# Kernel optimization log

Hardware: AMD Instinct MI355X
Metric: run time of the kernel (lower is better)

The kernel has to match this reference:

```python
import jax, jax.numpy as jnp
import numpy as np

B, S, H = 4, 1024, 1024
NH = 16
D = H // NH  # attention_head_size = 64
L = 9        # num_labels
MAXREL = 5
B_PERSON = 1
I_PERSON = 2
LN_EPS = 1e-5


def setup_inputs() -> dict:
    key = jax.random.key(0)
    ks = jax.random.split(key, 16)
    lin = lambda k, i, o: 0.02 * jax.random.normal(k, (i, o), jnp.float32)
    return {
        "sequence_output": jax.random.normal(ks[0], (B, S, H), jnp.float32),
        "Wq": lin(ks[1], H, H), "bq": jnp.zeros((H,), jnp.float32),
        "Wk": lin(ks[2], H, H), "bk": jnp.zeros((H,), jnp.float32),
        "Wv": lin(ks[3], H, H), "bv": jnp.zeros((H,), jnp.float32),
        "Wo": lin(ks[4], H, H), "bo": jnp.zeros((H,), jnp.float32),
        "ln_g": jnp.ones((H,), jnp.float32), "ln_b": jnp.zeros((H,), jnp.float32),
        "Ws": lin(ks[5], H, L), "bs": jnp.zeros((L,), jnp.float32),
        "entity_bias": 0.1 * jax.random.normal(ks[6], (L,), jnp.float32),
        "rel_pos_emb": jax.random.normal(ks[7], (2 * MAXREL + 1, D), jnp.float32),  # declared but unused in forward math, matching the torch module
    }


def reference(sequence_output, Wq, bq, Wk, bk, Wv, bv, Wo, bo, ln_g, ln_b, Ws, bs, entity_bias, rel_pos_emb):
    x = sequence_output  # [B,S,H]
    b, s, _ = x.shape

    def heads(t):  # [B,S,H] -> [B,NH,S,D]
        return t.reshape(b, s, NH, D).transpose(0, 2, 1, 3)

    q = heads(x @ Wq + bq)
    k = heads(x @ Wk + bk)
    v = heads(x @ Wv + bv)

    scores = jnp.einsum('bhqd,bhkd->bhqk', q, k)  # [B,NH,S,S]

    r = jnp.arange(s, dtype=jnp.float32)
    dist = jnp.abs(r[:, None] - r[None, :])                 # |i-j|, [S,S]
    pos_bias = jnp.exp(-0.1 * jnp.clip(dist, 0.0, float(MAXREL)))
    # torch order: (scores + pos_bias) / sqrt(D) + distance_mask
    scores = (scores + pos_bias) / np.sqrt(D) + (-0.1) * dist

    probs = jax.nn.softmax(scores, axis=-1)  # dropout is identity in eval
    ctx = jnp.einsum('bhqk,bhkd->bhqd', probs, v)
    ctx = ctx.transpose(0, 2, 1, 3).reshape(b, s, H)

    y = x + (ctx @ Wo + bo)  # residual
    mu = y.mean(-1, keepdims=True)
    var = y.var(-1, keepdims=True)
    yn = (y - mu) / jnp.sqrt(var + LN_EPS) * ln_g + ln_b

    span_logits = yn @ Ws + bs  # [B,S,L]
    # entity-bias loop: if argmax(span_logits[i,j-1]) == B-PERSON, add entity_bias[I-PERSON] twice to final[i,j,I-PERSON]
    prev_is_b = (jnp.argmax(span_logits[:, :-1, :], axis=-1) == B_PERSON).astype(span_logits.dtype)  # [B,S-1]
    final_logits = span_logits.at[:, 1:, I_PERSON].add(2.0 * entity_bias[I_PERSON] * prev_is_b)
    return final_logits
```

## Files before the change

kernel.cpp:

```cpp
#include <hip/hip_runtime.h>
#include <hip/hip_bf16.h>
#include <math.h>

typedef unsigned short ush;
typedef __attribute__((ext_vector_type(8))) _Float16 fragh;
typedef __attribute__((ext_vector_type(4))) _Float16 half4;
typedef __attribute__((ext_vector_type(4))) float f32x4;

#define S_   1024
#define H_   1024
#define NH_  16
#define D_   64
#define L_   9
#define MB_  (1048576ull)

__device__ __forceinline__ void load_lds16(const ush* g, const ush* l) {
  __builtin_amdgcn_global_load_lds(
      (const __attribute__((address_space(1))) void*)g,
      (__attribute__((address_space(3))) void*)l, 16, 0, 0);
}

__global__ __launch_bounds__(256) void cast_wT4(
    const float* W0, const float* W1, const float* W2, const float* W3,
    ush* T0, ush* T1, ush* T2, ush* T3) {
  __shared__ __align__(16) float Ls[64][68];
  const float* W = (blockIdx.z == 0) ? W0 : (blockIdx.z == 1) ? W1
                 : (blockIdx.z == 2) ? W2 : W3;
  ush* Th = (blockIdx.z == 0) ? T0 : (blockIdx.z == 1) ? T1
          : (blockIdx.z == 2) ? T2 : T3;
  const int tid = threadIdx.x;
  const int n0 = blockIdx.x * 64, k0 = blockIdx.y * 64;
#pragma unroll
  for (int it = 0; it < 4; it++) {
    int flat = tid + 256 * it;
    int row = flat >> 4, nc = (flat & 15) * 4;
    *(float4*)&Ls[row][nc] = *(const float4*)&W[(size_t)(k0 + row) * 1024 + n0 + nc];
  }
  __syncthreads();
#pragma unroll
  for (int it = 0; it < 2; it++) {
    int flat = tid + 256 * it;
    int nrow = flat >> 3, kc = (flat & 7) * 8;
    fragh v;
#pragma unroll
    for (int u = 0; u < 8; u++) v[u] = (_Float16)Ls[kc + u][nrow];
    *(fragh*)&Th[(size_t)(n0 + nrow) * 1024 + k0 + kc] = v;
  }
}

__global__ __launch_bounds__(256) void cast_x(
    const float* __restrict__ x, ush* __restrict__ xh) {
  const size_t i = ((size_t)blockIdx.x * 256 + threadIdx.x) * 8;
  float4 a = *(const float4*)&x[i];
  float4 b = *(const float4*)&x[i + 4];
  fragh v;
  v[0] = (_Float16)a.x; v[1] = (_Float16)a.y;
  v[2] = (_Float16)a.z; v[3] = (_Float16)a.w;
  v[4] = (_Float16)b.x; v[5] = (_Float16)b.y;
  v[6] = (_Float16)b.z; v[7] = (_Float16)b.w;
  *(fragh*)&xh[i] = v;
}

__global__ __launch_bounds__(256) void gemm_qkv(
    const ush* __restrict__ xh,
    const ush* __restrict__ Bq, const ush* __restrict__ Bk,
    const ush* __restrict__ Bv,
    const float* __restrict__ bq, const float* __restrict__ bk,
    const float* __restrict__ bv,
    ush* __restrict__ qh, ush* __restrict__ kh, ush* __restrict__ vT) {
  __shared__ __align__(16) ush As[2][128][32];
  __shared__ __align__(16) ush Bs[2][128][32];
  const int tid = threadIdx.x, lane = tid & 63, wave = tid >> 6;
  const int l15 = lane & 15, quad = lane >> 4;
  const int m0 = blockIdx.y * 128, n0 = blockIdx.x * 128;
  const int z = blockIdx.z;
  const ush* Bg = (z == 0) ? Bq : (z == 1) ? Bk : Bv;
  const float* bias = (z == 0) ? bq : (z == 1) ? bk : bv;
  ush* outp = (z == 0) ? qh : (z == 1) ? kh : vT;

  const int wm = (wave >> 1) * 64, wn = (wave & 1) * 64;

  f32x4 acc[4][4];
#pragma unroll
  for (int i = 0; i < 4; i++)
#pragma unroll
    for (int j = 0; j < 4; j++) acc[i][j] = (f32x4){0.f, 0.f, 0.f, 0.f};

  auto stage = [&](int bi, int k0) {
#pragma unroll
    for (int jj = 0; jj < 2; jj++) {
      const int call = wave * 2 + jj;
      const int c = call * 64 + lane;
      const int r = c >> 2, ch = c & 3;
      load_lds16(xh + (size_t)(m0 + r) * 1024 + k0 + ch * 8,
                 &As[bi][0][0] + (size_t)call * 512);
    }
#pragma unroll
    for (int jj = 0; jj < 2; jj++) {
      const int call = wave * 2 + jj;
      const int c = call * 64 + lane;
      const int r = c >> 2, ch = c & 3;
      load_lds16(Bg + (size_t)(n0 + r) * 1024 + k0 + ch * 8,
                 &Bs[bi][0][0] + (size_t)call * 512);
    }
  };

  auto compute = [&](int cur) {
    fragh a[4], b[2][2];
#pragma unroll
    for (int s = 0; s < 4; s++)
      a[s] = *(const fragh*)&As[cur][wm + s * 16 + l15][quad * 8];
#pragma unroll
    for (int t = 0; t < 4; t++) {
      fragh bt = *(const fragh*)&Bs[cur][wn + t * 16 + l15][quad * 8];
#pragma unroll
      for (int mi = 0; mi < 4; mi++)
        acc[mi][t] = __builtin_amdgcn_mfma_f32_16x16x32_f16(
            a[mi], bt, acc[mi][t], 0, 0, 0);
    }
    (void)b;
  };

  stage(0, 0);
#pragma unroll 1
  for (int t = 0; t < 31; ++t) {
    const int cur = t & 1;
    stage(cur ^ 1, (t + 1) << 5);
    __builtin_amdgcn_sched_barrier(0);
    asm volatile("s_waitcnt vmcnt(4)" ::: "memory");
    __builtin_amdgcn_sched_barrier(0);
    __builtin_amdgcn_s_barrier();
    compute(cur);
    __builtin_amdgcn_s_barrier();
  }
  __builtin_amdgcn_sched_barrier(0);
  asm volatile("s_waitcnt vmcnt(0)" ::: "memory");
  __builtin_amdgcn_sched_barrier(0);
  __builtin_amdgcn_s_barrier();
  compute(1);

#pragma unroll
  for (int mi = 0; mi < 4; mi++) {
    const int rbase = m0 + wm + mi * 16 + quad * 4;
    const int bb = rbase >> 10, ss = rbase & 1023;
#pragma unroll
    for (int ni = 0; ni < 4; ni++) {
      const int col = n0 + wn + ni * 16 + l15;
      const float bv_ = bias[col];
      const int hidx = col >> 6, d = col & 63;
      if (z == 2) {
        half4 p4;
        p4[0] = (_Float16)(acc[mi][ni][0] + bv_);
        p4[1] = (_Float16)(acc[mi][ni][1] + bv_);
        p4[2] = (_Float16)(acc[mi][ni][2] + bv_);
        p4[3] = (_Float16)(acc[mi][ni][3] + bv_);
        *(half4*)&outp[((size_t)(bb * NH_ + hidx) * D_ + d) * S_ + ss] = p4;
      } else {
#pragma unroll
        for (int r = 0; r < 4; r++) {
          const size_t o =
              ((size_t)(bb * NH_ + hidx) * S_ + (ss + r)) * D_ + d;
          *(_Float16*)&outp[o] = (_Float16)(acc[mi][ni][r] + bv_);
        }
      }
    }
  }
}

__global__ __launch_bounds__(256) void gemm_o(
    const ush* __restrict__ ctxh, const ush* __restrict__ Bo,
    const float* __restrict__ bo, const float* __restrict__ resid,
    float* __restrict__ outf) {
  __shared__ __align__(16) ush As[2][128][32];
  __shared__ __align__(16) ush Bs[2][64][32];
  const int tid = threadIdx.x, lane = tid & 63, wave = tid >> 6;
  const int l15 = lane & 15, quad = lane >> 4;
  const int m0 = blockIdx.y * 128, n0 = blockIdx.x * 64;
  const int wm = (wave >> 1) * 64, wn = (wave & 1) * 32;

  f32x4 acc[4][2];
#pragma unroll
  for (int i = 0; i < 4; i++)
#pragma unroll
    for (int j = 0; j < 2; j++) acc[i][j] = (f32x4){0.f, 0.f, 0.f, 0.f};

  auto stage = [&](int bi, int k0) {
#pragma unroll
    for (int jj = 0; jj < 2; jj++) {
      const int call = wave * 2 + jj;
      const int c = call * 64 + lane;
      const int r = c >> 2, ch = c & 3;
      load_lds16(ctxh + (size_t)(m0 + r) * 1024 + k0 + ch * 8,
                 &As[bi][0][0] + (size_t)call * 512);
    }
    {
      const int c = wave * 64 + lane;
      const int r = c >> 2, ch = c & 3;
      load_lds16(Bo + (size_t)(n0 + r) * 1024 + k0 + ch * 8,
                 &Bs[bi][0][0] + (size_t)wave * 512);
    }
  };

  auto compute = [&](int cur) {
    fragh a[4], b[2];
#pragma unroll
    for (int s = 0; s < 4; s++)
      a[s] = *(const fragh*)&As[cur][wm + s * 16 + l15][quad * 8];
#pragma unroll
    for (int t = 0; t < 2; t++)
      b[t] = *(const fragh*)&Bs[cur][wn + t * 16 + l15][quad * 8];
#pragma unroll
    for (int mi = 0; mi < 4; mi++)
#pragma unroll
      for (int ni = 0; ni < 2; ni++)
        acc[mi][ni] = __builtin_amdgcn_mfma_f32_16x16x32_f16(
            a[mi], b[ni], acc[mi][ni], 0, 0, 0);
  };

  stage(0, 0);
#pragma unroll 1
  for (int t = 0; t < 31; ++t) {
    const int cur = t & 1;
    stage(cur ^ 1, (t + 1) << 5);
    __builtin_amdgcn_sched_barrier(0);
    asm volatile("s_waitcnt vmcnt(3)" ::: "memory");
    __builtin_amdgcn_sched_barrier(0);
    __builtin_amdgcn_s_barrier();
    compute(cur);
    __builtin_amdgcn_s_barrier();
  }
  __builtin_amdgcn_sched_barrier(0);
  asm volatile("s_waitcnt vmcnt(0)" ::: "memory");
  __builtin_amdgcn_sched_barrier(0);
  __builtin_amdgcn_s_barrier();
  compute(1);

#pragma unroll
  for (int mi = 0; mi < 4; mi++) {
    const int rbase = m0 + wm + mi * 16 + quad * 4;
#pragma unroll
    for (int ni = 0; ni < 2; ni++) {
      const int col = n0 + wn + ni * 16 + l15;
      const float bv_ = bo[col];
#pragma unroll
      for (int r = 0; r < 4; r++) {
        const int m = rbase + r;
        outf[(size_t)m * 1024 + col] =
            acc[mi][ni][r] + bv_ + resid[(size_t)m * 1024 + col];
      }
    }
  }
}

__global__ __launch_bounds__(256) void attn2(
    const ush* __restrict__ qh, const ush* __restrict__ kh,
    const ush* __restrict__ vT, ush* __restrict__ ch) {
  __shared__ __align__(16) ush Kh[64][72];
  __shared__ __align__(16) ush VTs[64][72];
  __shared__ __align__(16) ush Pst[64][72];
  __shared__ float LUT[256];
  const int tid = threadIdx.x;
  const int lane = tid & 63, wave = tid >> 6;
  const int l15 = lane & 15, quad = lane >> 4;
  const int w16 = wave * 16;
  const int bh = blockIdx.y;
  const int b = bh >> 4, h = bh & 15;
  const int q0 = blockIdx.x * 64;

  const float K1 = 0.18033688011112042f;
  const float K2 = 0.14426950408889634f;
  {
    const float dd = (float)tid;
    LUT[tid] = __expf(-0.1f * fminf(dd, 5.0f)) * K1 - dd * K2
             - 2.8853900817779268f;
  }

  const size_t qrow = ((size_t)bh * S_ + q0 + w16 + l15) * D_;
  fragh a_h[2];
  a_h[0] = *(const fragh*)&qh[qrow + quad * 8];
  a_h[1] = *(const fragh*)&qh[qrow + 32 + quad * 8];

  f32x4 o[4];
  float lrow[4];
#pragma unroll
  for (int i = 0; i < 4; i++) {
    o[i] = (f32x4){0.f, 0.f, 0.f, 0.f};
    lrow[i] = 0.f;
  }

  const size_t kbase = (size_t)bh * S_ * D_;
  const size_t vbase = (size_t)bh * D_ * S_;

  const int jlo = (q0 > 128) ? q0 - 128 : 0;
  const int jend = (q0 + 192 < S_) ? q0 + 192 : S_;

  for (int j0 = jlo; j0 < jend; j0 += 64) {
    __syncthreads();
#pragma unroll
    for (int it = 0; it < 2; it++) {
      const int flat = tid + 256 * it;
      const int row = flat >> 3, dc = (flat & 7) * 8;
      *(uint4*)&Kh[row][dc] =
          *(const uint4*)&kh[kbase + (size_t)(j0 + row) * D_ + dc];
      *(uint4*)&VTs[row][dc] =
          *(const uint4*)&vT[vbase + (size_t)row * S_ + j0 + dc];
    }
    __syncthreads();

    f32x4 c4[4];
#pragma unroll
    for (int nt = 0; nt < 4; nt++) c4[nt] = (f32x4){0.f, 0.f, 0.f, 0.f};
#pragma unroll
    for (int kk = 0; kk < 2; kk++) {
#pragma unroll
      for (int nt = 0; nt < 4; nt++) {
        fragh bh_ = *(const fragh*)&Kh[nt * 16 + l15][kk * 32 + quad * 8];
        c4[nt] = __builtin_amdgcn_mfma_f32_16x16x32_f16(a_h[kk], bh_, c4[nt], 0, 0, 0);
      }
    }

    const int ib = q0 + w16 + quad * 4 - j0 - l15;
#pragma unroll
    for (int r = 0; r < 4; r++) {
#pragma unroll
      for (int nt = 0; nt < 4; nt++) {
        int di = ib + r - nt * 16;
        di = (di < 0) ? -di : di;
        const float sv = exp2f(fmaf(c4[nt][r], K1, LUT[di]));
        lrow[r] += sv;
        *(_Float16*)&Pst[w16 + quad * 4 + r][nt * 16 + l15] = (_Float16)sv;
      }
    }

    fragh pa[2];
    pa[0] = *(const fragh*)&Pst[w16 + l15][quad * 8];
    pa[1] = *(const fragh*)&Pst[w16 + l15][32 + quad * 8];
#pragma unroll
    for (int dt = 0; dt < 4; dt++) {
      fragh vb0 = *(const fragh*)&VTs[dt * 16 + l15][quad * 8];
      fragh vb1 = *(const fragh*)&VTs[dt * 16 + l15][32 + quad * 8];
      o[dt] = __builtin_amdgcn_mfma_f32_16x16x32_f16(pa[0], vb0, o[dt], 0, 0, 0);
      o[dt] = __builtin_amdgcn_mfma_f32_16x16x32_f16(pa[1], vb1, o[dt], 0, 0, 0);
    }
  }

#pragma unroll
  for (int r = 0; r < 4; r++) {
#pragma unroll
    for (int off = 1; off < 16; off <<= 1) lrow[r] += __shfl_xor(lrow[r], off);
    const float inv = 1.0f / lrow[r];
    const size_t rowp =
        ((size_t)(b * S_ + q0 + w16 + quad * 4 + r)) * H_ + h * 64;
#pragma unroll
    for (int dt = 0; dt < 4; dt++)
      *(_Float16*)&ch[rowp + dt * 16 + l15] = (_Float16)(o[dt][r] * inv);
  }
}

__global__ __launch_bounds__(256) void ln_span(
    const float* __restrict__ y, const float* __restrict__ g,
    const float* __restrict__ bta, const float* __restrict__ Wsp,
    const float* __restrict__ bs, float* __restrict__ logits) {
  const int row = blockIdx.x;
  const int tid = threadIdx.x, lane = tid & 63, wave = tid >> 6;
  const float* yr = y + (size_t)row * 1024;
  float vals[4], s = 0.f, s2 = 0.f;
#pragma unroll
  for (int i = 0; i < 4; i++) {
    float t = yr[tid + i * 256];
    vals[i] = t; s += t; s2 += t * t;
  }
#pragma unroll
  for (int off = 32; off; off >>= 1) {
    s += __shfl_xor(s, off);
    s2 += __shfl_xor(s2, off);
  }
  __shared__ float red[8];
  __shared__ float red9[4][12];
  if (lane == 0) { red[wave] = s; red[4 + wave] = s2; }
  __syncthreads();
  s = red[0] + red[1] + red[2] + red[3];
  s2 = red[4] + red[5] + red[6] + red[7];
  const float mu = s * (1.0f / 1024.0f);
  const float var = s2 * (1.0f / 1024.0f) - mu * mu;
  const float inv = rsqrtf(var + 1e-5f);

  float lg[9];
#pragma unroll
  for (int l = 0; l < 9; l++) lg[l] = 0.f;
#pragma unroll
  for (int i = 0; i < 4; i++) {
    const int hh = tid + i * 256;
    const float yn = (vals[i] - mu) * inv * g[hh] + bta[hh];
#pragma unroll
    for (int l = 0; l < 9; l++) lg[l] += yn * Wsp[hh * 9 + l];
  }
#pragma unroll
  for (int l = 0; l < 9; l++) {
#pragma unroll
    for (int off = 32; off; off >>= 1) lg[l] += __shfl_xor(lg[l], off);
  }
  if (lane == 0) {
#pragma unroll
    for (int l = 0; l < 9; l++) red9[wave][l] = lg[l];
  }
  __syncthreads();
  if (tid < 9) {
    logits[(size_t)row * 9 + tid] =
        red9[0][tid] + red9[1][tid] + red9[2][tid] + red9[3][tid] + bs[tid];
  }
}

__global__ __launch_bounds__(256) void final_kernel(
    const float* __restrict__ logits, const float* __restrict__ eb,
    float* __restrict__ out) {
  const int m = blockIdx.x * 256 + threadIdx.x;
  const int i = m & 1023;
  float cur[9];
#pragma unroll
  for (int l = 0; l < 9; l++) cur[l] = logits[(size_t)m * 9 + l];
  if (i > 0) {
    const float* prev = logits + (size_t)(m - 1) * 9;
    int am = 0;
    float best = prev[0];
#pragma unroll
    for (int l = 1; l < 9; l++) {
      float pv = prev[l];
      if (pv > best) { best = pv; am = l; }
    }
    if (am == 1) cur[2] += 2.0f * eb[2];
  }
#pragma unroll
  for (int l = 0; l < 9; l++) out[(size_t)m * 9 + l] = cur[l];
}

extern "C" void kernel_launch(void* const* d_in, const int* in_sizes, int n_in,
                              void* d_out, int out_size, void* d_ws, size_t ws_size,
                              hipStream_t stream) {
  const float* x    = (const float*)d_in[0];
  const float* Wq   = (const float*)d_in[1];
  const float* bq   = (const float*)d_in[2];
  const float* Wk   = (const float*)d_in[3];
  const float* bk   = (const float*)d_in[4];
  const float* Wv   = (const float*)d_in[5];
  const float* bv   = (const float*)d_in[6];
  const float* Wo   = (const float*)d_in[7];
  const float* bo   = (const float*)d_in[8];
  const float* ln_g = (const float*)d_in[9];
  const float* ln_b = (const float*)d_in[10];
  const float* Ws   = (const float*)d_in[11];
  const float* bs   = (const float*)d_in[12];
  const float* eb   = (const float*)d_in[13];
  float* out = (float*)d_out;
  char* W8 = (char*)d_ws;

  ush* WoT  = (ush*)(W8 + 0 * MB_);
  ush* WqT  = (ush*)(W8 + 2 * MB_);
  ush* WkT  = (ush*)(W8 + 4 * MB_);
  ush* WvT  = (ush*)(W8 + 6 * MB_);
  ush* xh   = (ush*)(W8 + 8 * MB_);
  ush* qh   = (ush*)(W8 + 16 * MB_);
  ush* kh   = (ush*)(W8 + 24 * MB_);
  ush* vT   = (ush*)(W8 + 32 * MB_);
  ush* ctxh = (ush*)(W8 + 40 * MB_);
  float* y_ws  = (float*)(W8 + 48 * MB_);
  float* lg_ws = (float*)(W8 + 16 * MB_);

  cast_wT4<<<dim3(16, 16, 4), 256, 0, stream>>>(
      Wq, Wk, Wv, Wo, WqT, WkT, WvT, WoT);
  cast_x<<<2048, 256, 0, stream>>>(x, xh);

  gemm_qkv<<<dim3(8, 32, 3), 256, 0, stream>>>(
      xh, WqT, WkT, WvT, bq, bk, bv, qh, kh, vT);
  attn2<<<dim3(16, 64), 256, 0, stream>>>(qh, kh, vT, ctxh);
  gemm_o<<<dim3(16, 32), 256, 0, stream>>>(ctxh, WoT, bo, x, y_ws);
  ln_span<<<4096, 256, 0, stream>>>(y_ws, ln_g, ln_b, Ws, bs, lg_ws);
  final_kernel<<<16, 256, 0, stream>>>(lg_ws, eb, out);
}
```

Measured before the change: 203.0 us.

## Merge prep casts, store residual output in fp16, warp-per-row LayerNorm, add setprio

The x cast, weight transposes and a new Ws transpose are combined into one prep launch. The output projection now writes the residual sum as fp16, halving the y traffic read by LayerNorm. LayerNorm+span is rewritten to one wave per row with vectorized loads and no block barriers. The attention MFMA sections are wrapped with s_setprio. Storing y in fp16 before LayerNorm slightly reduces precision.

```diff
diff --git a/kernel.cpp b/kernel.cpp
--- a/kernel.cpp
+++ b/kernel.cpp
@@ -20,45 +20,56 @@
       (__attribute__((address_space(3))) void*)l, 16, 0, 0);
 }
 
-__global__ __launch_bounds__(256) void cast_wT4(
+__global__ __launch_bounds__(256) void prep(
+    const float* __restrict__ x,
     const float* W0, const float* W1, const float* W2, const float* W3,
-    ush* T0, ush* T1, ush* T2, ush* T3) {
+    const float* __restrict__ Ws,
+    ush* __restrict__ xh, ush* T0, ush* T1, ush* T2, ush* T3,
+    float* __restrict__ WsT) {
   __shared__ __align__(16) float Ls[64][68];
-  const float* W = (blockIdx.z == 0) ? W0 : (blockIdx.z == 1) ? W1
-                 : (blockIdx.z == 2) ? W2 : W3;
-  ush* Th = (blockIdx.z == 0) ? T0 : (blockIdx.z == 1) ? T1
-          : (blockIdx.z == 2) ? T2 : T3;
+  const int bid = blockIdx.x;
   const int tid = threadIdx.x;
-  const int n0 = blockIdx.x * 64, k0 = blockIdx.y * 64;
+
+  if (bid < 2048) {
+    const size_t i = ((size_t)bid * 256 + tid) * 8;
+    float4 a = *(const float4*)&x[i];
+    float4 b = *(const float4*)&x[i + 4];
+    fragh v;
+    v[0] = (_Float16)a.x; v[1] = (_Float16)a.y;
+    v[2] = (_Float16)a.z; v[3] = (_Float16)a.w;
+    v[4] = (_Float16)b.x; v[5] = (_Float16)b.y;
+    v[6] = (_Float16)b.z; v[7] = (_Float16)b.w;
+    *(fragh*)&xh[i] = v;
+    return;
+  }
+  if (bid >= 3072) {
+    for (int idx = tid; idx < 1024 * 9; idx += 256) {
+      const int r = idx / 9, c = idx - r * 9;
+      WsT[c * 1024 + r] = Ws[idx];
+    }
+    return;
+  }
+  const int flat = bid - 2048;
+  const int wz = flat >> 8, wy = (flat >> 4) & 15, wx = flat & 15;
+  const float* W = (wz == 0) ? W0 : (wz == 1) ? W1 : (wz == 2) ? W2 : W3;
+  ush* Th = (wz == 0) ? T0 : (wz == 1) ? T1 : (wz == 2) ? T2 : T3;
+  const int n0 = wx * 64, k0 = wy * 64;
 #pragma unroll
   for (int it = 0; it < 4; it++) {
-    int flat = tid + 256 * it;
-    int row = flat >> 4, nc = (flat & 15) * 4;
+    int f = tid + 256 * it;
+    int row = f >> 4, nc = (f & 15) * 4;
     *(float4*)&Ls[row][nc] = *(const float4*)&W[(size_t)(k0 + row) * 1024 + n0 + nc];
   }
   __syncthreads();
 #pragma unroll
   for (int it = 0; it < 2; it++) {
-    int flat = tid + 256 * it;
-    int nrow = flat >> 3, kc = (flat & 7) * 8;
+    int f = tid + 256 * it;
+    int nrow = f >> 3, kc = (f & 7) * 8;
     fragh v;
 #pragma unroll
     for (int u = 0; u < 8; u++) v[u] = (_Float16)Ls[kc + u][nrow];
     *(fragh*)&Th[(size_t)(n0 + nrow) * 1024 + k0 + kc] = v;
   }
-}
-
-__global__ __launch_bounds__(256) void cast_x(
-    const float* __restrict__ x, ush* __restrict__ xh) {
-  const size_t i = ((size_t)blockIdx.x * 256 + threadIdx.x) * 8;
-  float4 a = *(const float4*)&x[i];
-  float4 b = *(const float4*)&x[i + 4];
-  fragh v;
-  v[0] = (_Float16)a.x; v[1] = (_Float16)a.y;
-  v[2] = (_Float16)a.z; v[3] = (_Float16)a.w;
-  v[4] = (_Float16)b.x; v[5] = (_Float16)b.y;
-  v[6] = (_Float16)b.z; v[7] = (_Float16)b.w;
-  *(fragh*)&xh[i] = v;
 }
 
 __global__ __launch_bounds__(256) void gemm_qkv(
@@ -106,7 +117,7 @@
   };
 
   auto compute = [&](int cur) {
-    fragh a[4], b[2][2];
+    fragh a[4];
 #pragma unroll
     for (int s = 0; s < 4; s++)
       a[s] = *(const fragh*)&As[cur][wm + s * 16 + l15][quad * 8];
@@ -118,7 +129,6 @@
         acc[mi][t] = __builtin_amdgcn_mfma_f32_16x16x32_f16(
             a[mi], bt, acc[mi][t], 0, 0, 0);
     }
-    (void)b;
   };
 
   stage(0, 0);
@@ -170,7 +180,7 @@
 __global__ __launch_bounds__(256) void gemm_o(
     const ush* __restrict__ ctxh, const ush* __restrict__ Bo,
     const float* __restrict__ bo, const float* __restrict__ resid,
-    float* __restrict__ outf) {
+    ush* __restrict__ yh) {
   __shared__ __align__(16) ush As[2][128][32];
   __shared__ __align__(16) ush Bs[2][64][32];
   const int tid = threadIdx.x, lane = tid & 63, wave = tid >> 6;
@@ -245,8 +255,9 @@
 #pragma unroll
       for (int r = 0; r < 4; r++) {
         const int m = rbase + r;
-        outf[(size_t)m * 1024 + col] =
+        const float val =
             acc[mi][ni][r] + bv_ + resid[(size_t)m * 1024 + col];
+        *(_Float16*)&yh[(size_t)m * 1024 + col] = (_Float16)val;
       }
     }
   }
@@ -310,6 +321,7 @@
     f32x4 c4[4];
 #pragma unroll
     for (int nt = 0; nt < 4; nt++) c4[nt] = (f32x4){0.f, 0.f, 0.f, 0.f};
+    __builtin_amdgcn_s_setprio(1);
 #pragma unroll
     for (int kk = 0; kk < 2; kk++) {
 #pragma unroll
@@ -318,6 +330,7 @@
         c4[nt] = __builtin_amdgcn_mfma_f32_16x16x32_f16(a_h[kk], bh_, c4[nt], 0, 0, 0);
       }
     }
+    __builtin_amdgcn_s_setprio(0);
 
     const int ib = q0 + w16 + quad * 4 - j0 - l15;
 #pragma unroll
@@ -335,6 +348,7 @@
     fragh pa[2];
     pa[0] = *(const fragh*)&Pst[w16 + l15][quad * 8];
     pa[1] = *(const fragh*)&Pst[w16 + l15][32 + quad * 8];
+    __builtin_amdgcn_s_setprio(1);
 #pragma unroll
     for (int dt = 0; dt < 4; dt++) {
       fragh vb0 = *(const fragh*)&VTs[dt * 16 + l15][quad * 8];
@@ -342,6 +356,7 @@
       o[dt] = __builtin_amdgcn_mfma_f32_16x16x32_f16(pa[0], vb0, o[dt], 0, 0, 0);
       o[dt] = __builtin_amdgcn_mfma_f32_16x16x32_f16(pa[1], vb1, o[dt], 0, 0, 0);
     }
+    __builtin_amdgcn_s_setprio(0);
   }
 
 #pragma unroll
@@ -358,56 +373,64 @@
 }
 
 __global__ __launch_bounds__(256) void ln_span(
-    const float* __restrict__ y, const float* __restrict__ g,
-    const float* __restrict__ bta, const float* __restrict__ Wsp,
+    const ush* __restrict__ yh, const float* __restrict__ g,
+    const float* __restrict__ bta, const float* __restrict__ WsT,
     const float* __restrict__ bs, float* __restrict__ logits) {
-  const int row = blockIdx.x;
   const int tid = threadIdx.x, lane = tid & 63, wave = tid >> 6;
-  const float* yr = y + (size_t)row * 1024;
-  float vals[4], s = 0.f, s2 = 0.f;
-#pragma unroll
-  for (int i = 0; i < 4; i++) {
-    float t = yr[tid + i * 256];
-    vals[i] = t; s += t; s2 += t * t;
-  }
+  const int row = blockIdx.x * 4 + wave;
+  const int h0 = lane * 16;
+  const ush* yr = yh + (size_t)row * 1024 + h0;
+
+  fragh v0 = *(const fragh*)yr;
+  fragh v1 = *(const fragh*)(yr + 8);
+  float v[16];
+#pragma unroll
+  for (int u = 0; u < 8; u++) { v[u] = (float)v0[u]; v[8 + u] = (float)v1[u]; }
+
+  float s = 0.f, s2 = 0.f;
+#pragma unroll
+  for (int u = 0; u < 16; u++) { s += v[u]; s2 += v[u] * v[u]; }
 #pragma unroll
   for (int off = 32; off; off >>= 1) {
     s += __shfl_xor(s, off);
     s2 += __shfl_xor(s2, off);
   }
-  __shared__ float red[8];
-  __shared__ float red9[4][12];
-  if (lane == 0) { red[wave] = s; red[4 + wave] = s2; }
-  __syncthreads();
-  s = red[0] + red[1] + red[2] + red[3];
-  s2 = red[4] + red[5] + red[6] + red[7];
   const float mu = s * (1.0f / 1024.0f);
   const float var = s2 * (1.0f / 1024.0f) - mu * mu;
   const float inv = rsqrtf(var + 1e-5f);
 
+  float yn[16];
+#pragma unroll
+  for (int i = 0; i < 4; i++) {
+    float4 gg = *(const float4*)&g[h0 + i * 4];
+    float4 bb = *(const float4*)&bta[h0 + i * 4];
+    yn[i * 4 + 0] = (v[i * 4 + 0] - mu) * inv * gg.x + bb.x;
+    yn[i * 4 + 1] = (v[i * 4 + 1] - mu) * inv * gg.y + bb.y;
+    yn[i * 4 + 2] = (v[i * 4 + 2] - mu) * inv * gg.z + bb.z;
+    yn[i * 4 + 3] = (v[i * 4 + 3] - mu) * inv * gg.w + bb.w;
+  }
+
   float lg[9];
 #pragma unroll
-  for (int l = 0; l < 9; l++) lg[l] = 0.f;
-#pragma unroll
-  for (int i = 0; i < 4; i++) {
-    const int hh = tid + i * 256;
-    const float yn = (vals[i] - mu) * inv * g[hh] + bta[hh];
-#pragma unroll
-    for (int l = 0; l < 9; l++) lg[l] += yn * Wsp[hh * 9 + l];
-  }
-#pragma unroll
   for (int l = 0; l < 9; l++) {
+    float acc = 0.f;
+#pragma unroll
+    for (int i = 0; i < 4; i++) {
+      float4 w4 = *(const float4*)&WsT[l * 1024 + h0 + i * 4];
+      acc += yn[i * 4 + 0] * w4.x + yn[i * 4 + 1] * w4.y +
+             yn[i * 4 + 2] * w4.z + yn[i * 4 + 3] * w4.w;
+    }
+    lg[l] = acc;
+  }
+#pragma unroll
+  for (int l = 0; l < 9; l++) {
 #pragma unroll
     for (int off = 32; off; off >>= 1) lg[l] += __shfl_xor(lg[l], off);
   }
   if (lane == 0) {
 #pragma unroll
-    for (int l = 0; l < 9; l++) red9[wave][l] = lg[l];
-  }
-  __syncthreads();
-  if (tid < 9) {
-    logits[(size_t)row * 9 + tid] =
-        red9[0][tid] + red9[1][tid] + red9[2][tid] + red9[3][tid] + bs[tid];
+    for (int l = 0; l < 9; l++)
+      logits[(size_t)row * 9 + l] = lg[l] + bs[l];
   }
 }
 
@@ -463,17 +486,17 @@
   ush* kh   = (ush*)(W8 + 24 * MB_);
   ush* vT   = (ush*)(W8 + 32 * MB_);
   ush* ctxh = (ush*)(W8 + 40 * MB_);
-  float* y_ws  = (float*)(W8 + 48 * MB_);
-  float* lg_ws = (float*)(W8 + 16 * MB_);
-
-  cast_wT4<<<dim3(16, 16, 4), 256, 0, stream>>>(
-      Wq, Wk, Wv, Wo, WqT, WkT, WvT, WoT);
-  cast_x<<<2048, 256, 0, stream>>>(x, xh);
+  ush* yh   = (ush*)(W8 + 48 * MB_);
+  float* lg_ws = (float*)(W8 + 56 * MB_);
+  float* WsT   = (float*)(W8 + 60 * MB_);
+
+  prep<<<3073, 256, 0, stream>>>(
+      x, Wq, Wk, Wv, Wo, Ws, xh, WqT, WkT, WvT, WoT, WsT);
 
   gemm_qkv<<<dim3(8, 32, 3), 256, 0, stream>>>(
       xh, WqT, WkT, WvT, bq, bk, bv, qh, kh, vT);
   attn2<<<dim3(16, 64), 256, 0, stream>>>(qh, kh, vT, ctxh);
-  gemm_o<<<dim3(16, 32), 256, 0, stream>>>(ctxh, WoT, bo, x, y_ws);
-  ln_span<<<4096, 256, 0, stream>>>(y_ws, ln_g, ln_b, Ws, bs, lg_ws);
+  gemm_o<<<dim3(16, 32), 256, 0, stream>>>(ctxh, WoT, bo, x, yh);
+  ln_span<<<1024, 256, 0, stream>>>(yh, ln_g, ln_b, WsT, bs, lg_ws);
   final_kernel<<<16, 256, 0, stream>>>(lg_ws, eb, out);
 }
```

Result: no change. 204.2 us (+0.6%).
